# Kernel optimization log

Measured on AMD Instinct MI355X. Metric: run time of the kernel, lower is better.

## Reference

```python
import jax, jax.numpy as jnp
import numpy as np

N_CODES = 8192
EMBED_DIM = 64
N_VOXELS = 32768


def setup_inputs() -> dict:
    key = jax.random.key(0)
    k1, k2 = jax.random.split(key)
    z_feats = jax.random.normal(k1, (N_VOXELS, EMBED_DIM), dtype=jnp.float32)
    embeddings = jax.random.normal(k2, (N_CODES, EMBED_DIM), dtype=jnp.float32)
    return {"z_feats": z_feats, "embeddings": embeddings}


def reference(z_feats, embeddings):
    # Pairwise squared euclidean distances: ||z||^2 - 2 z.e + ||e||^2  [N, K]
    z_sq = jnp.sum(z_feats * z_feats, axis=1, keepdims=True)        # [N, 1]
    e_sq = jnp.sum(embeddings * embeddings, axis=1)[None, :]        # [1, K]
    d2 = z_sq - 2.0 * jnp.einsum('nd,kd->nk', z_feats, embeddings) + e_sq
    # argmin is invariant under sqrt (cdist returns sqrt, but only indices are used)
    encoding_indices = jnp.argmin(d2, axis=1)                        # [N]
    quantized_feats = embeddings[encoding_indices]                   # [N, D]
    # commitment_loss = mse(z, sg(q));  vq_loss = mse(q, sg(z)) (gradient mode)
    commitment_loss = jnp.mean((z_feats - jax.lax.stop_gradient(quantized_feats)) ** 2)
    vq_loss = jnp.mean((quantized_feats - jax.lax.stop_gradient(z_feats)) ** 2)
    # straight-through estimator
    quantized_st = z_feats + jax.lax.stop_gradient(quantized_feats - z_feats)
    indices_out = encoding_indices[:, None].astype(jnp.float32)      # [N, 1]
    return quantized_st, vq_loss, commitment_loss, indices_out
```

## Files before the change

### kernel.cpp

```cpp
#include <hip/hip_runtime.h>
#include <float.h>

#define N_VOX 32768
#define N_CODES 8192
#define DIM 64

#define Q_OFF 0
#define VQ_OFF (N_VOX * DIM)
#define CM_OFF (VQ_OFF + 1)
#define IDX_OFF (VQ_OFF + 2)

#define WS_ACC 0
#define WS_ESQH 64
#define WS_IDX (WS_ESQH + N_CODES)
#define WS_EHI (WS_IDX + N_VOX)
#define WS_ELO (WS_EHI + N_CODES * DIM / 2)

typedef _Float16 half8 __attribute__((ext_vector_type(8)));
typedef float floatx4 __attribute__((ext_vector_type(4)));

__device__ inline void gld16(const void* g, void* l) {
  __builtin_amdgcn_global_load_lds(
      (const __attribute__((address_space(1))) unsigned int*)g,
      (__attribute__((address_space(3))) unsigned int*)l, 16, 0, 0);
}
__device__ inline void gld4(const void* g, void* l) {
  __builtin_amdgcn_global_load_lds(
      (const __attribute__((address_space(1))) unsigned int*)g,
      (__attribute__((address_space(3))) unsigned int*)l, 4, 0, 0);
}

__global__ __launch_bounds__(256) void k_cvt(const float* __restrict__ e,
                                             float* __restrict__ ws) {
  int gid = blockIdx.x * 256 + threadIdx.x;
  if (gid == 0) ws[WS_ACC] = 0.f;
  int row = gid >> 3, c = gid & 7;
  const float* src = e + (size_t)row * DIM + c * 8;
  float4 a = *(const float4*)src;
  float4 b = *(const float4*)(src + 4);
  float x[8] = {a.x, a.y, a.z, a.w, b.x, b.y, b.z, b.w};
  float s = 0.f;
  half8 hv, lv;
  #pragma unroll
  for (int j = 0; j < 8; ++j) {
    s += x[j] * x[j];
    _Float16 h = (_Float16)x[j];
    hv[j] = h;
    lv[j] = (_Float16)(x[j] - (float)h);
  }
  s += __shfl_xor(s, 1); s += __shfl_xor(s, 2); s += __shfl_xor(s, 4);
  if (c == 0) ws[WS_ESQH + row] = 0.5f * s;
  int p = (c + row) & 7;
  ((half8*)(ws + WS_EHI))[row * 8 + p] = hv;
  ((half8*)(ws + WS_ELO))[row * 8 + p] = lv;
}

__global__ __launch_bounds__(256, 2) void k_argmin(const float* __restrict__ z,
                                                   float* __restrict__ ws) {
  __shared__ __align__(16) _Float16 sBhi[128 * 64];
  __shared__ __align__(16) _Float16 sBlo[128 * 64];
  __shared__ float sEsq[128];
  __shared__ float sMval[128];
  __shared__ int   sMidx[128];

  const int tid  = threadIdx.x;
  const int lane = tid & 63;
  const int wave = tid >> 6;
  const int n16  = lane & 15;
  const int quad = lane >> 4;
  const int vgrp = wave >> 1;
  const int chalf = wave & 1;
  const int vb = blockIdx.x * 64;

  const char* ehi_b = (const char*)(ws + WS_EHI);
  const char* elo_b = (const char*)(ws + WS_ELO);
  const char* esq_b = (const char*)(ws + WS_ESQH);

  half8 ahi[2][2], alo[2][2];
  #pragma unroll
  for (int m = 0; m < 2; ++m)
    #pragma unroll
    for (int kc = 0; kc < 2; ++kc) {
      const float* src = z + (size_t)(vb + vgrp * 32 + m * 16 + n16) * DIM
                       + kc * 32 + quad * 8;
      float4 a = *(const float4*)src;
      float4 b = *(const float4*)(src + 4);
      float x[8] = {a.x, a.y, a.z, a.w, b.x, b.y, b.z, b.w};
      #pragma unroll
      for (int j = 0; j < 8; ++j) {
        _Float16 h = (_Float16)x[j];
        ahi[m][kc][j] = h;
        alo[m][kc][j] = (_Float16)(x[j] - (float)h);
      }
    }

  float bval[2][4]; int bidx[2][4];
  #pragma unroll
  for (int m = 0; m < 2; ++m)
    #pragma unroll
    for (int r = 0; r < 4; ++r) { bval[m][r] = FLT_MAX; bidx[m][r] = 0; }

  const int s0 = ((quad + n16) & 7) * 8;
  const int s1 = ((quad + 4 + n16) & 7) * 8;

  for (int ct = 0; ct < 64; ++ct) {
    const int cb = ct * 128;
    __syncthreads();
    #pragma unroll
    for (int r = 0; r < 4; ++r) {
      int off = (r * 4 + wave) * 1024;
      gld16(ehi_b + (size_t)cb * 128 + off + lane * 16, (char*)sBhi + off);
      gld16(elo_b + (size_t)cb * 128 + off + lane * 16, (char*)sBlo + off);
    }
    if (wave == 0) {
      gld4(esq_b + (size_t)cb * 4 + lane * 4, (char*)sEsq);
      gld4(esq_b + (size_t)cb * 4 + 256 + lane * 4, (char*)sEsq + 256);
    }
    __syncthreads();

    #pragma unroll
    for (int t = 0; t < 4; ++t) {
      const int rowb = chalf * 64 + t * 16;
      const int row = rowb + n16;
      half8 bh0 = *(const half8*)&sBhi[row * 64 + s0];
      half8 bh1 = *(const half8*)&sBhi[row * 64 + s1];
      half8 bl0 = *(const half8*)&sBlo[row * 64 + s0];
      half8 bl1 = *(const half8*)&sBlo[row * 64 + s1];
      float eh = sEsq[row];
      int code = cb + row;
      #pragma unroll
      for (int m = 0; m < 2; ++m) {
        floatx4 acc = {0.f, 0.f, 0.f, 0.f};
        acc = __builtin_amdgcn_mfma_f32_16x16x32_f16(ahi[m][0], bh0, acc, 0, 0, 0);
        acc = __builtin_amdgcn_mfma_f32_16x16x32_f16(ahi[m][1], bh1, acc, 0, 0, 0);
        acc = __builtin_amdgcn_mfma_f32_16x16x32_f16(ahi[m][0], bl0, acc, 0, 0, 0);
        acc = __builtin_amdgcn_mfma_f32_16x16x32_f16(ahi[m][1], bl1, acc, 0, 0, 0);
        acc = __builtin_amdgcn_mfma_f32_16x16x32_f16(alo[m][0], bh0, acc, 0, 0, 0);
        acc = __builtin_amdgcn_mfma_f32_16x16x32_f16(alo[m][1], bh1, acc, 0, 0, 0);
        acc = __builtin_amdgcn_mfma_f32_16x16x32_f16(alo[m][0], bl0, acc, 0, 0, 0);
        acc = __builtin_amdgcn_mfma_f32_16x16x32_f16(alo[m][1], bl1, acc, 0, 0, 0);
        #pragma unroll
        for (int r = 0; r < 4; ++r) {
          float tv = eh - acc[r];
          if (tv < bval[m][r]) { bval[m][r] = tv; bidx[m][r] = code; }
        }
      }
    }
  }

  #pragma unroll
  for (int m = 0; m < 2; ++m)
    #pragma unroll
    for (int r = 0; r < 4; ++r) {
      float v = bval[m][r]; int i = bidx[m][r];
      #pragma unroll
      for (int off = 1; off < 16; off <<= 1) {
        float ov = __shfl_xor(v, off);
        int   oi = __shfl_xor(i, off);
        if (ov < v || (ov == v && oi < i)) { v = ov; i = oi; }
      }
      if (n16 == 0) {
        int vox = vgrp * 32 + m * 16 + quad * 4 + r;
        sMval[chalf * 64 + vox] = v;
        sMidx[chalf * 64 + vox] = i;
      }
    }
  __syncthreads();
  if (tid < 64) {
    float v0 = sMval[tid], v1 = sMval[64 + tid];
    int   i0 = sMidx[tid], i1 = sMidx[64 + tid];
    bool p1 = (v1 < v0) || (v1 == v0 && i1 < i0);
    ((int*)ws)[WS_IDX + vb + tid] = p1 ? i1 : i0;
  }
}

__global__ __launch_bounds__(256) void k_out(const float* __restrict__ z,
                                             const float* __restrict__ e,
                                             float* __restrict__ ws,
                                             float* __restrict__ out) {
  const int tid = threadIdx.x;
  const int l4 = tid & 15;
  const int* idx_g = (const int*)ws + WS_IDX;
  float local = 0.f;
  int group = (blockIdx.x * 256 + tid) >> 4;
  for (int n = group; n < N_VOX; n += 4096) {
    int idx = idx_g[n];
    float4 e4 = *(const float4*)(e + (size_t)idx * DIM + l4 * 4);
    float4 z4 = *(const float4*)(z + (size_t)n * DIM + l4 * 4);
    *(float4*)(out + Q_OFF + (size_t)n * DIM + l4 * 4) = e4;
    float dx = z4.x - e4.x, dy = z4.y - e4.y, dz = z4.z - e4.z, dw = z4.w - e4.w;
    local += dx * dx + dy * dy + dz * dz + dw * dw;
    if (l4 == 0) out[IDX_OFF + n] = (float)idx;
  }
  #pragma unroll
  for (int off = 32; off; off >>= 1) local += __shfl_xor(local, off);
  __shared__ float wsum[4];
  if ((tid & 63) == 0) wsum[tid >> 6] = local;
  __syncthreads();
  if (tid == 0) atomicAdd(ws + WS_ACC, wsum[0] + wsum[1] + wsum[2] + wsum[3]);
}

__global__ void k_fin(const float* __restrict__ ws, float* __restrict__ out) {
  float m = ws[WS_ACC] * (1.0f / (float)(N_VOX * DIM));
  out[VQ_OFF] = m;
  out[CM_OFF] = m;
}

extern "C" void kernel_launch(void* const* d_in, const int* in_sizes, int n_in,
                              void* d_out, int out_size, void* d_ws, size_t ws_size,
                              hipStream_t stream) {
  const float* z = (const float*)d_in[0];
  const float* e = (const float*)d_in[1];
  float* out = (float*)d_out;
  float* ws = (float*)d_ws;

  k_cvt<<<(N_CODES * 8) / 256, 256, 0, stream>>>(e, ws);
  k_argmin<<<N_VOX / 64, 256, 0, stream>>>(z, ws);
  k_out<<<256, 256, 0, stream>>>(z, e, ws, out);
  k_fin<<<1, 1, 0, stream>>>(ws, out);
}
```

Baseline: 199.4 us.

## Double-buffer codebook tiles, drop lo*lo MFMA term, fuse output and loss into argmin

Result: faster. 189.3 us (-5.1%).

```diff
diff --git a/kernel.cpp b/kernel.cpp
--- a/kernel.cpp
+++ b/kernel.cpp
@@ -11,6 +11,7 @@
 #define IDX_OFF (VQ_OFF + 2)
 
 #define WS_ACC 0
+#define WS_CNT 1
 #define WS_ESQH 64
 #define WS_IDX (WS_ESQH + N_CODES)
 #define WS_EHI (WS_IDX + N_VOX)
@@ -33,7 +34,10 @@
 __global__ __launch_bounds__(256) void k_cvt(const float* __restrict__ e,
                                              float* __restrict__ ws) {
   int gid = blockIdx.x * 256 + threadIdx.x;
-  if (gid == 0) ws[WS_ACC] = 0.f;
+  if (gid == 0) {
+    ws[WS_ACC] = 0.f;
+    ((int*)ws)[WS_CNT] = 0;
+  }
   int row = gid >> 3, c = gid & 7;
   const float* src = e + (size_t)row * DIM + c * 8;
   float4 a = *(const float4*)src;
@@ -56,12 +60,16 @@
 }
 
 __global__ __launch_bounds__(256, 2) void k_argmin(const float* __restrict__ z,
-                                                   float* __restrict__ ws) {
-  __shared__ __align__(16) _Float16 sBhi[128 * 64];
-  __shared__ __align__(16) _Float16 sBlo[128 * 64];
-  __shared__ float sEsq[128];
+                                                   const float* __restrict__ e,
+                                                   float* __restrict__ ws,
+                                                   float* __restrict__ out) {
+  __shared__ __align__(16) _Float16 sBhi[2][128 * 64];
+  __shared__ __align__(16) _Float16 sBlo[2][128 * 64];
+  __shared__ float sEsq[2][128];
   __shared__ float sMval[128];
   __shared__ int   sMidx[128];
+  __shared__ int   sWin[64];
+  __shared__ float sWsum[4];
 
   const int tid  = threadIdx.x;
   const int lane = tid & 63;
@@ -103,30 +111,40 @@
   const int s0 = ((quad + n16) & 7) * 8;
   const int s1 = ((quad + 4 + n16) & 7) * 8;
 
-  for (int ct = 0; ct < 64; ++ct) {
-    const int cb = ct * 128;
-    __syncthreads();
+  auto stage = [&](int buf, int ct) {
+    const size_t cbb = (size_t)ct * 128 * 128;
     #pragma unroll
     for (int r = 0; r < 4; ++r) {
       int off = (r * 4 + wave) * 1024;
-      gld16(ehi_b + (size_t)cb * 128 + off + lane * 16, (char*)sBhi + off);
-      gld16(elo_b + (size_t)cb * 128 + off + lane * 16, (char*)sBlo + off);
+      gld16(ehi_b + cbb + off + lane * 16, (char*)sBhi[buf] + off);
+      gld16(elo_b + cbb + off + lane * 16, (char*)sBlo[buf] + off);
     }
     if (wave == 0) {
-      gld4(esq_b + (size_t)cb * 4 + lane * 4, (char*)sEsq);
-      gld4(esq_b + (size_t)cb * 4 + 256 + lane * 4, (char*)sEsq + 256);
-    }
-    __syncthreads();
+      gld4(esq_b + (size_t)ct * 512 + lane * 4, (char*)sEsq[buf]);
+      gld4(esq_b + (size_t)ct * 512 + 256 + lane * 4, (char*)sEsq[buf] + 256);
+    }
+  };
+
+  stage(0, 0);
+  __syncthreads();
+
+  for (int ct = 0; ct < 64; ++ct) {
+    const int cur = ct & 1;
+    if (ct < 63) stage(cur ^ 1, ct + 1);
+
+    const _Float16* bhiP = sBhi[cur];
+    const _Float16* bloP = sBlo[cur];
+    const float*    esqP = sEsq[cur];
+    const int cb = ct * 128;
 
     #pragma unroll
     for (int t = 0; t < 4; ++t) {
-      const int rowb = chalf * 64 + t * 16;
-      const int row = rowb + n16;
-      half8 bh0 = *(const half8*)&sBhi[row * 64 + s0];
-      half8 bh1 = *(const half8*)&sBhi[row * 64 + s1];
-      half8 bl0 = *(const half8*)&sBlo[row * 64 + s0];
-      half8 bl1 = *(const half8*)&sBlo[row * 64 + s1];
-      float eh = sEsq[row];
+      const int row = chalf * 64 + t * 16 + n16;
+      half8 bh0 = *(const half8*)&bhiP[row * 64 + s0];
+      half8 bh1 = *(const half8*)&bhiP[row * 64 + s1];
+      half8 bl0 = *(const half8*)&bloP[row * 64 + s0];
+      half8 bl1 = *(const half8*)&bloP[row * 64 + s1];
+      float eh = esqP[row];
       int code = cb + row;
       #pragma unroll
       for (int m = 0; m < 2; ++m) {
@@ -137,8 +155,6 @@
         acc = __builtin_amdgcn_mfma_f32_16x16x32_f16(ahi[m][1], bl1, acc, 0, 0, 0);
         acc = __builtin_amdgcn_mfma_f32_16x16x32_f16(alo[m][0], bh0, acc, 0, 0, 0);
         acc = __builtin_amdgcn_mfma_f32_16x16x32_f16(alo[m][1], bh1, acc, 0, 0, 0);
-        acc = __builtin_amdgcn_mfma_f32_16x16x32_f16(alo[m][0], bl0, acc, 0, 0, 0);
-        acc = __builtin_amdgcn_mfma_f32_16x16x32_f16(alo[m][1], bl1, acc, 0, 0, 0);
         #pragma unroll
         for (int r = 0; r < 4; ++r) {
           float tv = eh - acc[r];
@@ -146,6 +162,7 @@
         }
       }
     }
+    __syncthreads();
   }
 
   #pragma unroll
@@ -166,44 +183,50 @@
       }
     }
   __syncthreads();
+
   if (tid < 64) {
     float v0 = sMval[tid], v1 = sMval[64 + tid];
     int   i0 = sMidx[tid], i1 = sMidx[64 + tid];
     bool p1 = (v1 < v0) || (v1 == v0 && i1 < i0);
-    ((int*)ws)[WS_IDX + vb + tid] = p1 ? i1 : i0;
-  }
-}
-
-__global__ __launch_bounds__(256) void k_out(const float* __restrict__ z,
-                                             const float* __restrict__ e,
-                                             float* __restrict__ ws,
-                                             float* __restrict__ out) {
-  const int tid = threadIdx.x;
-  const int l4 = tid & 15;
-  const int* idx_g = (const int*)ws + WS_IDX;
-  float local = 0.f;
-  int group = (blockIdx.x * 256 + tid) >> 4;
-  for (int n = group; n < N_VOX; n += 4096) {
-    int idx = idx_g[n];
-    float4 e4 = *(const float4*)(e + (size_t)idx * DIM + l4 * 4);
-    float4 z4 = *(const float4*)(z + (size_t)n * DIM + l4 * 4);
-    *(float4*)(out + Q_OFF + (size_t)n * DIM + l4 * 4) = e4;
-    float dx = z4.x - e4.x, dy = z4.y - e4.y, dz = z4.z - e4.z, dw = z4.w - e4.w;
-    local += dx * dx + dy * dy + dz * dz + dw * dw;
-    if (l4 == 0) out[IDX_OFF + n] = (float)idx;
-  }
-  #pragma unroll
-  for (int off = 32; off; off >>= 1) local += __shfl_xor(local, off);
-  __shared__ float wsum[4];
-  if ((tid & 63) == 0) wsum[tid >> 6] = local;
+    int w = p1 ? i1 : i0;
+    sWin[tid] = w;
+    out[IDX_OFF + vb + tid] = (float)w;
+  }
   __syncthreads();
-  if (tid == 0) atomicAdd(ws + WS_ACC, wsum[0] + wsum[1] + wsum[2] + wsum[3]);
-}
-
-__global__ void k_fin(const float* __restrict__ ws, float* __restrict__ out) {
-  float m = ws[WS_ACC] * (1.0f / (float)(N_VOX * DIM));
-  out[VQ_OFF] = m;
-  out[CM_OFF] = m;
+
+  {
+    const int vox = tid >> 2;
+    const int dc = (tid & 3) * 16;
+    const int gi = sWin[vox];
+    const float* er = e + (size_t)gi * DIM + dc;
+    const float* zr = z + (size_t)(vb + vox) * DIM + dc;
+    float* qr = out + Q_OFF + (size_t)(vb + vox) * DIM + dc;
+    float local = 0.f;
+    #pragma unroll
+    for (int j = 0; j < 4; ++j) {
+      float4 e4 = *(const float4*)(er + j * 4);
+      float4 z4 = *(const float4*)(zr + j * 4);
+      *(float4*)(qr + j * 4) = e4;
+      float dx = z4.x - e4.x, dy = z4.y - e4.y, dz = z4.z - e4.z, dw = z4.w - e4.w;
+      local += dx * dx + dy * dy + dz * dz + dw * dw;
+    }
+    #pragma unroll
+    for (int off = 32; off; off >>= 1) local += __shfl_xor(local, off);
+    if ((tid & 63) == 0) sWsum[wave] = local;
+    __syncthreads();
+    if (tid == 0) {
+      float bs = sWsum[0] + sWsum[1] + sWsum[2] + sWsum[3];
+      atomicAdd(ws + WS_ACC, bs);
+      __threadfence();
+      int done = atomicAdd((int*)ws + WS_CNT, 1);
+      if (done == (int)gridDim.x - 1) {
+        float s = atomicAdd(ws + WS_ACC, 0.f);
+        float mv = s * (1.0f / (float)(N_VOX * DIM));
+        out[VQ_OFF] = mv;
+        out[CM_OFF] = mv;
+      }
+    }
+  }
 }
 
 extern "C" void kernel_launch(void* const* d_in, const int* in_sizes, int n_in,
@@ -215,7 +238,5 @@
   float* ws = (float*)d_ws;
 
   k_cvt<<<(N_CODES * 8) / 256, 256, 0, stream>>>(e, ws);
-  k_argmin<<<N_VOX / 64, 256, 0, stream>>>(z, ws);
-  k_out<<<256, 256, 0, stream>>>(z, e, ws, out);
-  k_fin<<<1, 1, 0, stream>>>(ws, out);
-}
+  k_argmin<<<N_VOX / 64, 256, 0, stream>>>(z, e, ws, out);
+}
```
